# Kernel tuning notes

Hardware: AMD Instinct MI355X
Metric: run time of the kernel (lower is better)

Reference implementation:

```python
import jax, jax.numpy as jnp
import numpy as np

B, S, E = 2, 2048, 2048
H, HD = 32, 64          # n_heads, head_dim
KV, REP = 8, 4          # n_kv_head, n_kv_head_rep (H == KV*REP)
NEG = -1e9


def setup_inputs() -> dict:
    key = jax.random.key(0)
    ks = jax.random.split(key, 6)
    x = jax.random.normal(ks[0], (B, S, E), dtype=jnp.float32)
    # Llama RoPE tables: angles[p, i] = p / 10000^(2i/HD)
    inv_freq = 1.0 / (10000.0 ** (jnp.arange(0, HD, 2, dtype=jnp.float32) / HD))
    angles = jnp.arange(S, dtype=jnp.float32)[:, None] * inv_freq[None, :]  # [S, HD/2]
    cos, sin = jnp.cos(angles), jnp.sin(angles)
    # causal additive mask [S, S]
    mask = jnp.where(jnp.tril(jnp.ones((S, S), dtype=bool)), 0.0, NEG).astype(jnp.float32)
    sc = 0.02
    wq = jax.random.normal(ks[1], (E, H * HD), dtype=jnp.float32) * sc
    wk = jax.random.normal(ks[2], (E, KV * HD), dtype=jnp.float32) * sc
    wv = jax.random.normal(ks[3], (E, KV * HD), dtype=jnp.float32) * sc
    wo = jax.random.normal(ks[4], (H * HD, E), dtype=jnp.float32) * sc
    return {"x": x, "cos": cos, "sin": sin, "mask": mask,
            "wq": wq, "wk": wk, "wv": wv, "wo": wo, "start_pos": 0}


def _rope(t, cos, sin):
    # t: [B, S, h, HD]; rotate consecutive pairs (Llama complex convention)
    tp = t.reshape(t.shape[:-1] + (HD // 2, 2))
    t1, t2 = tp[..., 0], tp[..., 1]
    c = cos[None, :, None, :]
    s = sin[None, :, None, :]
    out = jnp.stack([t1 * c - t2 * s, t1 * s + t2 * c], axis=-1)
    return out.reshape(t.shape)


def reference(x, cos, sin, mask, wq, wk, wv, wo, start_pos):
    b, s, _ = x.shape
    q = (x @ wq).reshape(b, s, H, HD)
    k = (x @ wk).reshape(b, s, KV, HD)
    v = (x @ wv).reshape(b, s, KV, HD)
    q = _rope(q, cos, sin)
    k = _rope(k, cos, sin)
    # KV-cache: with start_pos=0 and full-seq prefill, the cache slice
    # [:, :start_pos+s] is exactly the freshly written k/v, so use them directly.
    # Grouped attention without materializing repeated K/V:
    # q -> [b, KV, REP, s, HD]; k,v -> [b, KV, s, HD]
    qg = q.transpose(0, 2, 1, 3).reshape(b, KV, REP, s, HD)
    kg = k.transpose(0, 2, 1, 3)
    vg = v.transpose(0, 2, 1, 3)
    scale = 1.0 / jnp.sqrt(jnp.float32(HD))
    scores = jnp.einsum('bgrqd,bgkd->bgrqk', qg, kg) * scale + mask
    attn = jax.nn.softmax(scores, axis=-1)
    og = jnp.einsum('bgrqk,bgkd->bgrqd', attn, vg)     # [b, KV, REP, s, HD]
    out = og.reshape(b, H, s, HD).transpose(0, 2, 1, 3).reshape(b, s, H * HD)
    return out @ wo
```

## Files before the change

kernel.cpp:

```cpp
#include <hip/hip_runtime.h>
#include <stdint.h>

#define S_LEN 2048
#define NTOK  4096
#define EMB   2048
#define NHEAD 32
#define HDIM  64
#define NKVH  8

typedef __bf16 bf16x8 __attribute__((ext_vector_type(8)));
typedef float  f32x4  __attribute__((ext_vector_type(4)));

#define AS1 __attribute__((address_space(1)))
#define AS3 __attribute__((address_space(3)))

#if __has_builtin(__builtin_amdgcn_exp2f)
#define EXP2(x) __builtin_amdgcn_exp2f(x)
#else
#define EXP2(x) exp2f(x)
#endif

#define QSCALE 0.1803368867f

__device__ __forceinline__ uint16_t f2bf(float f) {
  uint32_t u = __float_as_uint(f);
  u += 0x7fffu + ((u >> 16) & 1u);
  return (uint16_t)(u >> 16);
}
__device__ __forceinline__ float bf2f(uint16_t h) {
  return __uint_as_float(((uint32_t)h) << 16);
}
__device__ __forceinline__ void gld16(const void* g, void* l) {
  __builtin_amdgcn_global_load_lds((const AS1 uint32_t*)g, (AS3 uint32_t*)l, 16, 0, 0);
}
__device__ __forceinline__ f32x4 mfma16(bf16x8 a, bf16x8 b, f32x4 c) {
  return __builtin_amdgcn_mfma_f32_16x16x32_bf16(a, b, c, 0, 0, 0);
}

__global__ void k_cvt(const float* __restrict__ in, uint16_t* __restrict__ out) {
  int i = (blockIdx.x * 256 + threadIdx.x) * 4;
  float4 v = *(const float4*)(in + i);
  ushort4 o;
  o.x = f2bf(v.x); o.y = f2bf(v.y); o.z = f2bf(v.z); o.w = f2bf(v.w);
  *(ushort4*)(out + i) = o;
}

__global__ void k_transpose(const float* __restrict__ in, uint16_t* __restrict__ out,
                            int R, int C) {
  __shared__ float tile[32][33];
  int c0 = blockIdx.x * 32, r0 = blockIdx.y * 32;
  int tx = threadIdx.x & 31, ty = threadIdx.x >> 5;
#pragma unroll
  for (int j = 0; j < 32; j += 8)
    tile[ty + j][tx] = in[(size_t)(r0 + ty + j) * C + c0 + tx];
  __syncthreads();
#pragma unroll
  for (int j = 0; j < 32; j += 8)
    out[(size_t)(c0 + ty + j) * R + r0 + tx] = f2bf(tile[tx][ty + j]);
}

__global__ void k_transpose_v(const uint16_t* __restrict__ qkv, uint16_t* __restrict__ out) {
  __shared__ uint16_t tile[32][33];
  int s0 = blockIdx.x * 32, hd0 = blockIdx.y * 32, bh = blockIdx.z;
  int b = bh >> 3, kvh = bh & 7;
  int tx = threadIdx.x & 31, ty = threadIdx.x >> 5;
#pragma unroll
  for (int j = 0; j < 32; j += 8)
    tile[ty + j][tx] =
        qkv[((size_t)b * S_LEN + s0 + ty + j) * 3072 + 2560 + kvh * 64 + hd0 + tx];
  __syncthreads();
#pragma unroll
  for (int j = 0; j < 32; j += 8)
    out[((size_t)bh * 64 + hd0 + ty + j) * S_LEN + s0 + tx] = tile[tx][ty + j];
}

template <int N_REP, typename OUT_T>
__global__ __launch_bounds__(512, 1) void k_gemm256(
    const uint16_t* __restrict__ A, const uint16_t* __restrict__ BT,
    OUT_T* __restrict__ C, int M, int N, int K) {
  constexpr int LDSH = 16384 + N_REP * 4096;
  __shared__ uint16_t lds[2][LDSH];
  const int tid = threadIdx.x, lane = tid & 63, w = tid >> 6;
  const int wm = w >> 2, wn = w & 3;
  const int l16 = lane & 15, lg = lane >> 4;
  const int nbn = N / (N_REP * 64);
  const int nwg = gridDim.x, cpx = nwg >> 3;
  const int swz = ((int)blockIdx.x & 7) * cpx + ((int)blockIdx.x >> 3);
  const int bm = (swz / nbn) * 256, bn = (swz % nbn) * (N_REP * 64);

  f32x4 acc[8][N_REP] = {};

  const int srow = tid >> 3, sslot = tid & 7;
  const int schunk = (sslot ^ (srow & 7)) * 8;
  const uint16_t* Ag = A + (size_t)(bm + srow) * K + schunk;
  const uint16_t* Bg = BT + (size_t)(bn + srow) * K + schunk;

  auto stageA = [&](int d, int r, int k0) {
    gld16(Ag + (size_t)r * 64 * K + k0, &lds[d][r * 4096 + tid * 8]);
  };
  auto stageB = [&](int d, int r, int k0) {
    gld16(Bg + (size_t)r * 64 * K + k0, &lds[d][16384 + r * 4096 + tid * 8]);
  };
  auto lda = [&](int d, int mf, int s) -> bf16x8 {
    int row = wm * 128 + mf * 16 + l16;
    int slot = (s * 4 + lg) ^ (row & 7);
    return *(const bf16x8*)(&lds[d][row * 64 + slot * 8]);
  };
  auto ldb = [&](int d, int nf, int s) -> bf16x8 {
    int row = wn * (N_REP * 16) + nf * 16 + l16;
    int slot = (s * 4 + lg) ^ (row & 7);
    return *(const bf16x8*)(&lds[d][16384 + row * 64 + slot * 8]);
  };

  const int NT = K >> 6;
#pragma unroll
  for (int r = 0; r < 4; ++r) stageA(0, r, 0);
#pragma unroll
  for (int r = 0; r < N_REP; ++r) stageB(0, r, 0);
#pragma unroll
  for (int r = 0; r < 4; ++r) if (1 < NT) stageA(1, r, 64);
  asm volatile("s_waitcnt vmcnt(4)" ::: "memory");
  __builtin_amdgcn_s_barrier();

  for (int kt = 0; kt < NT; ++kt) {
    const int cur = kt & 1;
    const int nk0 = (kt + 1) << 6, nnk0 = (kt + 2) << 6;
    const bool m1 = (kt + 1 < NT), m2 = (kt + 2 < NT);
    bf16x8 a[4][2], a2[4][2], b[N_REP][2];
#pragma unroll
    for (int mi = 0; mi < 4; ++mi) { a[mi][0] = lda(cur, mi, 0); a[mi][1] = lda(cur, mi, 1); }
#pragma unroll
    for (int ni = 0; ni < N_REP; ++ni) { b[ni][0] = ldb(cur, ni, 0); b[ni][1] = ldb(cur, ni, 1); }
    if (m1) {
#pragma unroll
      for (int r = 0; r < N_REP; ++r) stageB(cur ^ 1, r, nk0);
    }
    __builtin_amdgcn_s_barrier();
    asm volatile("s_waitcnt lgkmcnt(0)" ::: "memory");
    __builtin_amdgcn_sched_barrier(0);
    __builtin_amdgcn_s_setprio(1);
#pragma unroll
    for (int mi = 0; mi < 4; ++mi)
#pragma unroll
      for (int ni = 0; ni < 2; ++ni) {
        acc[mi][ni] = mfma16(a[mi][0], b[ni][0], acc[mi][ni]);
        acc[mi][ni] = mfma16(a[mi][1], b[ni][1], acc[mi][ni]);
      }
    __builtin_amdgcn_s_setprio(0);
    __builtin_amdgcn_s_barrier();
#pragma unroll
    for (int mi = 0; mi < 4; ++mi) { a2[mi][0] = lda(cur, 4 + mi, 0); a2[mi][1] = lda(cur, 4 + mi, 1); }
    __builtin_amdgcn_s_barrier();
    asm volatile("s_waitcnt lgkmcnt(0)" ::: "memory");
    __builtin_amdgcn_sched_barrier(0);
    __builtin_amdgcn_s_setprio(1);
    if constexpr (N_REP == 3) {
#pragma unroll
      for (int mi = 0; mi < 4; ++mi) {
        acc[mi][2] = mfma16(a[mi][0], b[2][0], acc[mi][2]);
        acc[mi][2] = mfma16(a[mi][1], b[2][1], acc[mi][2]);
      }
    }
#pragma unroll
    for (int mi = 0; mi < 4; ++mi) {
      acc[4 + mi][0] = mfma16(a2[mi][0], b[0][0], acc[4 + mi][0]);
      acc[4 + mi][0] = mfma16(a2[mi][1], b[0][1], acc[4 + mi][0]);
    }
    __builtin_amdgcn_s_setprio(0);
    __builtin_amdgcn_s_barrier();
    if (m2) {
#pragma unroll
      for (int r = 0; r < 4; ++r) stageA(cur, r, nnk0);
    }
    __builtin_amdgcn_s_setprio(1);
#pragma unroll
    for (int mi = 0; mi < 4; ++mi)
#pragma unroll
      for (int ni = 1; ni < N_REP; ++ni) {
        acc[4 + mi][ni] = mfma16(a2[mi][0], b[ni][0], acc[4 + mi][ni]);
        acc[4 + mi][ni] = mfma16(a2[mi][1], b[ni][1], acc[4 + mi][ni]);
      }
    __builtin_amdgcn_s_setprio(0);
    if (m2) { asm volatile("s_waitcnt vmcnt(4)" ::: "memory"); }
    else    { asm volatile("s_waitcnt vmcnt(0)" ::: "memory"); }
    __builtin_amdgcn_s_barrier();
  }
#pragma unroll
  for (int mf = 0; mf < 8; ++mf)
#pragma unroll
    for (int nf = 0; nf < N_REP; ++nf)
#pragma unroll
      for (int r = 0; r < 4; ++r) {
        int row = bm + wm * 128 + mf * 16 + lg * 4 + r;
        int col = bn + wn * (N_REP * 16) + nf * 16 + l16;
        float v = acc[mf][nf][r];
        if constexpr (sizeof(OUT_T) == 4) C[(size_t)row * N + col] = v;
        else                              C[(size_t)row * N + col] = f2bf(v);
      }
}

__global__ void k_rope(const uint16_t* __restrict__ qkv, const float* __restrict__ cosT,
                       const float* __restrict__ sinT, uint16_t* __restrict__ qb,
                       uint16_t* __restrict__ kb) {
  int idx = blockIdx.x * 256 + threadIdx.x;
  int row = idx / 1280;
  int col = (idx - row * 1280) * 2;
  int s = row & (S_LEN - 1);
  uint32_t vv = *(const uint32_t*)(qkv + (size_t)row * 3072 + col);
  float t1 = bf2f((uint16_t)vv), t2 = bf2f((uint16_t)(vv >> 16));
  int i = (col & 63) >> 1;
  if (col < 2048) {
    float c = cosT[s * 32 + i] * QSCALE, sn = sinT[s * 32 + i] * QSCALE;
    uint32_t o = (uint32_t)f2bf(t1 * c - t2 * sn) | ((uint32_t)f2bf(t1 * sn + t2 * c) << 16);
    *(uint32_t*)(qb + (size_t)row * 2048 + col) = o;
  } else {
    int cc = col - 2048;
    float c = cosT[s * 32 + i], sn = sinT[s * 32 + i];
    uint32_t o = (uint32_t)f2bf(t1 * c - t2 * sn) | ((uint32_t)f2bf(t1 * sn + t2 * c) << 16);
    *(uint32_t*)(kb + (size_t)row * 512 + cc) = o;
  }
}

template <bool MASKED>
__device__ __forceinline__ void tile_compute(
    const uint16_t* Kc, const uint16_t* Vc, const bf16x8 qf[2][2], bf16x8 onesv,
    int l16, int lg, int kv0, int qb0,
    float m_r[2], f32x4 lacc[2], f32x4 acc[2][4]) {
  f32x4 st[2][4] = {};
  __builtin_amdgcn_s_setprio(1);
#pragma unroll
  for (int c = 0; c < 4; ++c) {
    int row = c * 16 + l16, sw = row & 7;
    bf16x8 ka  = *(const bf16x8*)(Kc + row * 64 + ((lg ^ sw) * 8));
    bf16x8 kb2 = *(const bf16x8*)(Kc + row * 64 + (((4 | lg) ^ sw) * 8));
#pragma unroll
    for (int qc = 0; qc < 2; ++qc) {
      st[qc][c] = mfma16(ka,  qf[qc][0], st[qc][c]);
      st[qc][c] = mfma16(kb2, qf[qc][1], st[qc][c]);
    }
  }
  __builtin_amdgcn_s_setprio(0);
  bf16x8 pu[2][2];
#pragma unroll
  for (int qc = 0; qc < 2; ++qc) {
    const int qrow = qb0 + qc * 16 + l16;
    float sv[4][4];
#pragma unroll
    for (int c = 0; c < 4; ++c)
#pragma unroll
      for (int r = 0; r < 4; ++r) {
        float s = st[qc][c][r];
        if (MASKED && (kv0 + c * 16 + lg * 4 + r > qrow)) s = -1e30f;
        sv[c][r] = s;
      }
    float m0 = fmaxf(fmaxf(sv[0][0], sv[0][1]), fmaxf(sv[0][2], sv[0][3]));
    float m1 = fmaxf(fmaxf(sv[1][0], sv[1][1]), fmaxf(sv[1][2], sv[1][3]));
    float m2 = fmaxf(fmaxf(sv[2][0], sv[2][1]), fmaxf(sv[2][2], sv[2][3]));
    float m3 = fmaxf(fmaxf(sv[3][0], sv[3][1]), fmaxf(sv[3][2], sv[3][3]));
    float mx = fmaxf(fmaxf(m0, m1), fmaxf(m2, m3));
    mx = fmaxf(mx, __shfl_xor(mx, 16));
    mx = fmaxf(mx, __shfl_xor(mx, 32));
    if (!__all(mx - m_r[qc] <= 8.0f)) {
      float m_new = fmaxf(m_r[qc], mx);
      float alpha = EXP2(m_r[qc] - m_new);
      float al[4];
#pragma unroll
      for (int r = 0; r < 4; ++r) al[r] = __shfl(alpha, lg * 4 + r);
#pragma unroll
      for (int n = 0; n < 4; ++n)
#pragma unroll
        for (int r = 0; r < 4; ++r) acc[qc][n][r] *= al[r];
#pragma unroll
      for (int r = 0; r < 4; ++r) lacc[qc][r] *= al[r];
      m_r[qc] = m_new;
    }
    float pf[4][4];
#pragma unroll
    for (int c = 0; c < 4; ++c)
#pragma unroll
      for (int r = 0; r < 4; ++r)
        pf[c][r] = EXP2(sv[c][r] - m_r[qc]);
#pragma unroll
    for (int cc = 0; cc < 2; ++cc)
#pragma unroll
      for (int e = 0; e < 8; ++e)
        ((__bf16*)&pu[qc][cc])[e] = (__bf16)pf[cc * 2 + (e >> 2)][e & 3];
  }
  __builtin_amdgcn_s_setprio(1);
#pragma unroll
  for (int cc = 0; cc < 2; ++cc) {
    lacc[0] = mfma16(pu[0][cc], onesv, lacc[0]);
    lacc[1] = mfma16(pu[1][cc], onesv, lacc[1]);
#pragma unroll
    for (int n = 0; n < 4; ++n) {
      int row = n * 16 + l16, sw2 = row & 7;
      int k0 = cc * 32 + lg * 4, k1 = k0 + 16;
      const char* base = (const char*)Vc + row * 128;
      union { uint64_t q[2]; bf16x8 v; } vu;
      vu.q[0] = *(const uint64_t*)(base + (((k0 >> 3) ^ sw2) << 4) + ((k0 & 7) << 1));
      vu.q[1] = *(const uint64_t*)(base + (((k1 >> 3) ^ sw2) << 4) + ((k1 & 7) << 1));
      acc[0][n] = mfma16(pu[0][cc], vu.v, acc[0][n]);
      acc[1][n] = mfma16(pu[1][cc], vu.v, acc[1][n]);
    }
  }
  __builtin_amdgcn_s_setprio(0);
}

__global__ __launch_bounds__(256, 3) void k_flash(
    const uint16_t* __restrict__ Qb, const uint16_t* __restrict__ Kb,
    const uint16_t* __restrict__ VT, uint16_t* __restrict__ Ob) {
  __shared__ uint16_t Ks[3][4096];
  __shared__ uint16_t Vs[3][4096];
  const int j = 63 - ((int)blockIdx.x >> 4);
  const int gb = blockIdx.x & 15;
  const int g = gb & 7, b = gb >> 3;
  const int tid = threadIdx.x, lane = tid & 63, w = tid >> 6;
  const int l16 = lane & 15, lg = lane >> 4;
  const int h = g * 4 + w;
  const int qb0 = j * 32;

  bf16x8 qf[2][2];
#pragma unroll
  for (int qc = 0; qc < 2; ++qc) {
    const size_t tokq = (size_t)b * S_LEN + qb0 + qc * 16 + l16;
    qf[qc][0] = *(const bf16x8*)(Qb + tokq * 2048 + h * 64 + lg * 8);
    qf[qc][1] = *(const bf16x8*)(Qb + tokq * 2048 + h * 64 + 32 + lg * 8);
  }
  bf16x8 onesv;
#pragma unroll
  for (int e = 0; e < 8; ++e) ((__bf16*)&onesv)[e] = (__bf16)1.0f;

  const int srow = tid >> 3, shc = tid & 7;
  const int swz = (shc ^ (srow & 7)) * 8;
  const uint16_t* Kg = Kb + ((size_t)b * S_LEN + srow) * 512 + g * 64 + swz;
  const uint16_t* Vg = VT + ((size_t)(b * 8 + g) * 64 + srow) * S_LEN + swz;

  float m_r[2] = {-1e30f, -1e30f};
  f32x4 lacc[2] = {};
  f32x4 acc[2][4] = {};
  const int nt = (j >> 1) + 1;

  auto stage = [&](int t, int buf) {
    const size_t kv0 = (size_t)t * 64;
    uint16_t* kd = &Ks[buf][tid * 8];
    uint16_t* vd = &Vs[buf][tid * 8];
    gld16(Kg + kv0 * 512, kd);
    gld16(Kg + (kv0 + 32) * 512, kd + 2048);
    gld16(Vg + kv0, vd);
    gld16(Vg + kv0 + (size_t)32 * S_LEN, vd + 2048);
  };

  stage(0, 0);
  stage(nt > 1 ? 1 : 0, 1);

  int cur = 0;
  for (int t = 0; t < nt; ++t) {
    asm volatile("s_waitcnt vmcnt(4)" ::: "memory");
    __builtin_amdgcn_s_barrier();
    {
      int ts = t + 2 < nt ? t + 2 : nt - 1;
      int bufn = cur + 2; if (bufn >= 3) bufn -= 3;
      stage(ts, bufn);
    }
    if (t == nt - 1)
      tile_compute<true >(Ks[cur], Vs[cur], qf, onesv, l16, lg, t * 64, qb0, m_r, lacc, acc);
    else
      tile_compute<false>(Ks[cur], Vs[cur], qf, onesv, l16, lg, t * 64, qb0, m_r, lacc, acc);
    cur = cur + 1 < 3 ? cur + 1 : 0;
  }
#pragma unroll
  for (int qc = 0; qc < 2; ++qc) {
    float li[4];
#pragma unroll
    for (int r = 0; r < 4; ++r) li[r] = 1.0f / lacc[qc][r];
#pragma unroll
    for (int n = 0; n < 4; ++n)
#pragma unroll
      for (int r = 0; r < 4; ++r) {
        int qo = qb0 + qc * 16 + lg * 4 + r;
        Ob[((size_t)b * S_LEN + qo) * 2048 + h * 64 + n * 16 + l16] =
            f2bf(acc[qc][n][r] * li[r]);
      }
  }
}

extern "C" void kernel_launch(void* const* d_in, const int* in_sizes, int n_in,
                              void* d_out, int out_size, void* d_ws, size_t ws_size,
                              hipStream_t stream) {
  const float* x    = (const float*)d_in[0];
  const float* cosT = (const float*)d_in[1];
  const float* sinT = (const float*)d_in[2];
  const float* wq   = (const float*)d_in[4];
  const float* wk   = (const float*)d_in[5];
  const float* wv   = (const float*)d_in[6];
  const float* wo   = (const float*)d_in[7];
  float* out = (float*)d_out;

  char* ws = (char*)d_ws;
  size_t off = 0;
  auto alloc = [&](size_t bytes) {
    void* p = ws + off;
    off += (bytes + 255) & ~(size_t)255;
    return p;
  };
  uint16_t* xb   = (uint16_t*)alloc((size_t)NTOK * EMB * 2);
  uint16_t* wT   = (uint16_t*)alloc((size_t)3072 * 2048 * 2);
  uint16_t* woT  = (uint16_t*)alloc((size_t)2048 * 2048 * 2);
  uint16_t* qkvb = (uint16_t*)alloc((size_t)NTOK * 3072 * 2);
  uint16_t* qb   = (uint16_t*)alloc((size_t)NTOK * 2048 * 2);
  uint16_t* kb   = (uint16_t*)alloc((size_t)NTOK * 512 * 2);
  uint16_t* vT   = (uint16_t*)alloc((size_t)NTOK * 512 * 2);
  uint16_t* ob   = xb;

  k_cvt<<<(NTOK * EMB) / 1024, 256, 0, stream>>>(x, xb);
  k_transpose<<<dim3(64, 64), 256, 0, stream>>>(wq, wT, 2048, 2048);
  k_transpose<<<dim3(16, 64), 256, 0, stream>>>(wk, wT + (size_t)2048 * 2048, 2048, 512);
  k_transpose<<<dim3(16, 64), 256, 0, stream>>>(wv, wT + (size_t)2560 * 2048, 2048, 512);
  k_transpose<<<dim3(64, 64), 256, 0, stream>>>(wo, woT, 2048, 2048);

  k_gemm256<3, uint16_t><<<256, 512, 0, stream>>>(xb, wT, qkvb, 4096, 3072, 2048);
  k_rope<<<(NTOK * 1280) / 256, 256, 0, stream>>>(qkvb, cosT, sinT, qb, kb);
  k_transpose_v<<<dim3(64, 2, 16), 256, 0, stream>>>(qkvb, vT);
  k_flash<<<dim3(1024), 256, 0, stream>>>(qb, kb, vT, ob);
  k_gemm256<2, float><<<256, 512, 0, stream>>>(ob, woT, out, 4096, 2048, 2048);
}
```

Baseline: 182.5 us.

## Shrink GEMM block tile to 128 rows with 256 threads, two blocks per CU

The projection GEMM kernel changes from a 256-row tile run by 512 threads (one block per CU) to a 128-row tile run by 256 threads, with launch bounds allowing two blocks per CU. Each wave now covers 64 rows by twice as many columns, the LDS staging and fragment indexing are reworked to match, and the grid doubles to 512 blocks. The aim is better occupancy and load balance over the 256 CUs, with two co-resident blocks hiding each other's barriers. The cost is lower reuse of the A operand per block, so more global and LDS traffic per FLOP.

```diff
diff --git a/kernel.cpp b/kernel.cpp
--- a/kernel.cpp
+++ b/kernel.cpp
@@ -75,20 +75,21 @@
 }
 
 template <int N_REP, typename OUT_T>
-__global__ __launch_bounds__(512, 1) void k_gemm256(
+__global__ __launch_bounds__(256, 2) void k_gemm128(
     const uint16_t* __restrict__ A, const uint16_t* __restrict__ BT,
     OUT_T* __restrict__ C, int M, int N, int K) {
-  constexpr int LDSH = 16384 + N_REP * 4096;
+  constexpr int NF = 2 * N_REP;
+  constexpr int LDSH = 8192 + N_REP * 4096;
   __shared__ uint16_t lds[2][LDSH];
   const int tid = threadIdx.x, lane = tid & 63, w = tid >> 6;
-  const int wm = w >> 2, wn = w & 3;
+  const int wm = w >> 1, wn = w & 1;
   const int l16 = lane & 15, lg = lane >> 4;
   const int nbn = N / (N_REP * 64);
   const int nwg = gridDim.x, cpx = nwg >> 3;
   const int swz = ((int)blockIdx.x & 7) * cpx + ((int)blockIdx.x >> 3);
-  const int bm = (swz / nbn) * 256, bn = (swz % nbn) * (N_REP * 64);
-
-  f32x4 acc[8][N_REP] = {};
+  const int bm = (swz / nbn) * 128, bn = (swz % nbn) * (N_REP * 64);
+
+  f32x4 acc[4][NF] = {};
 
   const int srow = tid >> 3, sslot = tid & 7;
   const int schunk = (sslot ^ (srow & 7)) * 8;
@@ -96,27 +97,27 @@
   const uint16_t* Bg = BT + (size_t)(bn + srow) * K + schunk;
 
   auto stageA = [&](int d, int r, int k0) {
-    gld16(Ag + (size_t)r * 64 * K + k0, &lds[d][r * 4096 + tid * 8]);
+    gld16(Ag + (size_t)r * 32 * K + k0, &lds[d][r * 2048 + tid * 8]);
   };
   auto stageB = [&](int d, int r, int k0) {
-    gld16(Bg + (size_t)r * 64 * K + k0, &lds[d][16384 + r * 4096 + tid * 8]);
+    gld16(Bg + (size_t)r * 32 * K + k0, &lds[d][8192 + r * 2048 + tid * 8]);
   };
   auto lda = [&](int d, int mf, int s) -> bf16x8 {
-    int row = wm * 128 + mf * 16 + l16;
+    int row = wm * 64 + mf * 16 + l16;
     int slot = (s * 4 + lg) ^ (row & 7);
     return *(const bf16x8*)(&lds[d][row * 64 + slot * 8]);
   };
   auto ldb = [&](int d, int nf, int s) -> bf16x8 {
-    int row = wn * (N_REP * 16) + nf * 16 + l16;
+    int row = wn * (N_REP * 32) + nf * 16 + l16;
     int slot = (s * 4 + lg) ^ (row & 7);
-    return *(const bf16x8*)(&lds[d][16384 + row * 64 + slot * 8]);
+    return *(const bf16x8*)(&lds[d][8192 + row * 64 + slot * 8]);
   };
 
   const int NT = K >> 6;
 #pragma unroll
   for (int r = 0; r < 4; ++r) stageA(0, r, 0);
 #pragma unroll
-  for (int r = 0; r < N_REP; ++r) stageB(0, r, 0);
+  for (int r = 0; r < 2 * N_REP; ++r) stageB(0, r, 0);
 #pragma unroll
   for (int r = 0; r < 4; ++r) if (1 < NT) stageA(1, r, 64);
   asm volatile("s_waitcnt vmcnt(4)" ::: "memory");
@@ -126,46 +127,41 @@
     const int cur = kt & 1;
     const int nk0 = (kt + 1) << 6, nnk0 = (kt + 2) << 6;
     const bool m1 = (kt + 1 < NT), m2 = (kt + 2 < NT);
-    bf16x8 a[4][2], a2[4][2], b[N_REP][2];
-#pragma unroll
-    for (int mi = 0; mi < 4; ++mi) { a[mi][0] = lda(cur, mi, 0); a[mi][1] = lda(cur, mi, 1); }
-#pragma unroll
-    for (int ni = 0; ni < N_REP; ++ni) { b[ni][0] = ldb(cur, ni, 0); b[ni][1] = ldb(cur, ni, 1); }
+    bf16x8 a[2][2], a2[2][2], b[NF][2];
+#pragma unroll
+    for (int mi = 0; mi < 2; ++mi) { a[mi][0] = lda(cur, mi, 0); a[mi][1] = lda(cur, mi, 1); }
+#pragma unroll
+    for (int ni = 0; ni < NF; ++ni) { b[ni][0] = ldb(cur, ni, 0); b[ni][1] = ldb(cur, ni, 1); }
     if (m1) {
 #pragma unroll
-      for (int r = 0; r < N_REP; ++r) stageB(cur ^ 1, r, nk0);
+      for (int r = 0; r < 2 * N_REP; ++r) stageB(cur ^ 1, r, nk0);
     }
     __builtin_amdgcn_s_barrier();
     asm volatile("s_waitcnt lgkmcnt(0)" ::: "memory");
     __builtin_amdgcn_sched_barrier(0);
     __builtin_amdgcn_s_setprio(1);
 #pragma unroll
-    for (int mi = 0; mi < 4; ++mi)
-#pragma unroll
-      for (int ni = 0; ni < 2; ++ni) {
+    for (int mi = 0; mi < 2; ++mi)
+#pragma unroll
+      for (int ni = 0; ni < NF; ++ni) {
         acc[mi][ni] = mfma16(a[mi][0], b[ni][0], acc[mi][ni]);
         acc[mi][ni] = mfma16(a[mi][1], b[ni][1], acc[mi][ni]);
       }
     __builtin_amdgcn_s_setprio(0);
     __builtin_amdgcn_s_barrier();
 #pragma unroll
-    for (int mi = 0; mi < 4; ++mi) { a2[mi][0] = lda(cur, 4 + mi, 0); a2[mi][1] = lda(cur, 4 + mi, 1); }
+    for (int mi = 0; mi < 2; ++mi) { a2[mi][0] = lda(cur, 2 + mi, 0); a2[mi][1] = lda(cur, 2 + mi, 1); }
     __builtin_amdgcn_s_barrier();
     asm volatile("s_waitcnt lgkmcnt(0)" ::: "memory");
     __builtin_amdgcn_sched_barrier(0);
     __builtin_amdgcn_s_setprio(1);
-    if constexpr (N_REP == 3) {
-#pragma unroll
-      for (int mi = 0; mi < 4; ++mi) {
-        acc[mi][2] = mfma16(a[mi][0], b[2][0], acc[mi][2]);
-        acc[mi][2] = mfma16(a[mi][1], b[2][1], acc[mi][2]);
-      }
-    }
-#pragma unroll
-    for (int mi = 0; mi < 4; ++mi) {
-      acc[4 + mi][0] = mfma16(a2[mi][0], b[0][0], acc[4 + mi][0]);
-      acc[4 + mi][0] = mfma16(a2[mi][1], b[0][1], acc[4 + mi][0]);
-    }
+#pragma unroll
+    for (int mi = 0; mi < 2; ++mi)
+#pragma unroll
+      for (int ni = 0; ni < N_REP; ++ni) {
+        acc[2 + mi][ni] = mfma16(a2[mi][0], b[ni][0], acc[2 + mi][ni]);
+        acc[2 + mi][ni] = mfma16(a2[mi][1], b[ni][1], acc[2 + mi][ni]);
+      }
     __builtin_amdgcn_s_setprio(0);
     __builtin_amdgcn_s_barrier();
     if (m2) {
@@ -174,11 +170,11 @@
     }
     __builtin_amdgcn_s_setprio(1);
 #pragma unroll
-    for (int mi = 0; mi < 4; ++mi)
-#pragma unroll
-      for (int ni = 1; ni < N_REP; ++ni) {
-        acc[4 + mi][ni] = mfma16(a2[mi][0], b[ni][0], acc[4 + mi][ni]);
-        acc[4 + mi][ni] = mfma16(a2[mi][1], b[ni][1], acc[4 + mi][ni]);
+    for (int mi = 0; mi < 2; ++mi)
+#pragma unroll
+      for (int ni = N_REP; ni < NF; ++ni) {
+        acc[2 + mi][ni] = mfma16(a2[mi][0], b[ni][0], acc[2 + mi][ni]);
+        acc[2 + mi][ni] = mfma16(a2[mi][1], b[ni][1], acc[2 + mi][ni]);
       }
     __builtin_amdgcn_s_setprio(0);
     if (m2) { asm volatile("s_waitcnt vmcnt(4)" ::: "memory"); }
@@ -186,13 +182,13 @@
     __builtin_amdgcn_s_barrier();
   }
 #pragma unroll
-  for (int mf = 0; mf < 8; ++mf)
-#pragma unroll
-    for (int nf = 0; nf < N_REP; ++nf)
+  for (int mf = 0; mf < 4; ++mf)
+#pragma unroll
+    for (int nf = 0; nf < NF; ++nf)
 #pragma unroll
       for (int r = 0; r < 4; ++r) {
-        int row = bm + wm * 128 + mf * 16 + lg * 4 + r;
-        int col = bn + wn * (N_REP * 16) + nf * 16 + l16;
+        int row = bm + wm * 64 + mf * 16 + lg * 4 + r;
+        int col = bn + wn * (N_REP * 32) + nf * 16 + l16;
         float v = acc[mf][nf][r];
         if constexpr (sizeof(OUT_T) == 4) C[(size_t)row * N + col] = v;
         else                              C[(size_t)row * N + col] = f2bf(v);
@@ -418,9 +414,9 @@
   k_transpose<<<dim3(16, 64), 256, 0, stream>>>(wv, wT + (size_t)2560 * 2048, 2048, 512);
   k_transpose<<<dim3(64, 64), 256, 0, stream>>>(wo, woT, 2048, 2048);
 
-  k_gemm256<3, uint16_t><<<256, 512, 0, stream>>>(xb, wT, qkvb, 4096, 3072, 2048);
+  k_gemm128<3, uint16_t><<<512, 256, 0, stream>>>(xb, wT, qkvb, 4096, 3072, 2048);
   k_rope<<<(NTOK * 1280) / 256, 256, 0, stream>>>(qkvb, cosT, sinT, qb, kb);
   k_transpose_v<<<dim3(64, 2, 16), 256, 0, stream>>>(qkvb, vT);
   k_flash<<<dim3(1024), 256, 0, stream>>>(qb, kb, vT, ob);
-  k_gemm256<2, float><<<256, 512, 0, stream>>>(ob, woT, out, 4096, 2048, 2048);
-}
+  k_gemm128<2, float><<<512, 256, 0, stream>>>(ob, woT, out, 4096, 2048, 2048);
+}
```

After: 179.5 us. About the same (-1.7%).
